# Kernel optimization log

Hardware: AMD Instinct MI355X
Metric: run time of the kernel (lower is better)

The kernel has to match this reference:

```python
import jax, jax.numpy as jnp
import numpy as np

C = 256          # n_channels
D = 32           # head_dim
HEADS = C // D   # 8 heads in the MLA block
EXP = 4          # MBConv expansion
EPS = 1e-15      # attention epsilon
BN_EPS = 1e-5    # BatchNorm eps (eval mode, mean=0, var=1)
BN_SCALE = 1.0 / np.sqrt(1.0 + BN_EPS)


def _hswish(x):
    return x * jnp.clip(x + 3.0, 0.0, 6.0) * (1.0 / 6.0)


def _dwconv(x, w, pad):
    # depthwise conv, NCHW, weight (Cout,1,k,k), groups = Cout
    return jax.lax.conv_general_dilated(
        x, w, (1, 1), [(pad, pad), (pad, pad)],
        feature_group_count=w.shape[0],
        dimension_numbers=('NCHW', 'OIHW', 'NCHW'))


def _bn(x, gamma, beta):
    # eval-mode BN with running_mean=0, running_var=1
    return (gamma * BN_SCALE)[None, :, None, None] * x + beta[None, :, None, None]


def setup_inputs() -> dict:
    key = jax.random.key(0)
    ks = jax.random.split(key, 16)
    s = 0.05
    return {
        'x': jax.random.normal(ks[0], (8, C, 64, 64), jnp.float32),
        'W_qkv': jax.random.normal(ks[1], (3 * C, C), jnp.float32) * s,
        'W_dw5': jax.random.normal(ks[2], (3 * C, 1, 5, 5), jnp.float32) * s,
        'W_pw': jax.random.normal(ks[3], (3 * HEADS, D, D), jnp.float32) * s,
        'W_proj': jax.random.normal(ks[4], (C, 2 * C), jnp.float32) * s,
        'g_proj': jnp.ones((C,), jnp.float32),
        'b_proj': jnp.zeros((C,), jnp.float32),
        'W_e': jax.random.normal(ks[5], (EXP * C, C), jnp.float32) * s,
        'b_e': jax.random.normal(ks[6], (EXP * C,), jnp.float32) * s,
        'W_dw3': jax.random.normal(ks[7], (EXP * C, 1, 3, 3), jnp.float32) * s,
        'b_dw3': jax.random.normal(ks[8], (EXP * C,), jnp.float32) * s,
        'W_p': jax.random.normal(ks[9], (C, EXP * C), jnp.float32) * s,
        'g_p': jnp.ones((C,), jnp.float32),
        'b_p': jnp.zeros((C,), jnp.float32),
    }


def reference(x, W_qkv, W_dw5, W_pw, W_proj, g_proj, b_proj,
              W_e, b_e, W_dw3, b_dw3, W_p, g_p, b_p):
    B, _, H, W = x.shape
    # --- LightweightMLABlock ---
    qkv = jnp.einsum('oi,bihw->bohw', W_qkv, x)                 # (B,3C,H,W)
    # multi-scale aggregator: dw5x5 -> grouped 1x1 (groups=3*HEADS, 32x32 each)
    ag = _dwconv(qkv, W_dw5, 2)
    ag = ag.reshape(B, 3 * HEADS, D, H, W)
    ag = jnp.einsum('ged,bgdhw->bgehw', W_pw, ag).reshape(B, 3 * C, H, W)
    qkv_cat = jnp.concatenate([qkv, ag], axis=1)                # (B,6C,H,W)
    # ReLU linear attention (H*W=4096 > D=32 -> linear branch)
    N = H * W
    t = qkv_cat.reshape(B, 2 * HEADS, 3 * D, N)
    q = jax.nn.relu(t[:, :, :D])
    k = jax.nn.relu(t[:, :, D:2 * D])
    v = t[:, :, 2 * D:]
    vpad = jnp.concatenate([v, jnp.ones((B, 2 * HEADS, 1, N), v.dtype)], axis=2)
    vk = jnp.einsum('bhdn,bhen->bhde', vpad, k)                 # (B,h,D+1,D)
    out = jnp.einsum('bhde,bhen->bhdn', vk, q)                  # (B,h,D+1,N)
    out = out[:, :, :D] / (out[:, :, D:] + EPS)
    att = out.reshape(B, 2 * C, H, W)
    proj = _bn(jnp.einsum('oi,bihw->bohw', W_proj, att), g_proj, b_proj)
    y = proj + x                                                # attention residual
    # --- MobileBottleneckBlock ---
    e = _hswish(jnp.einsum('oi,bihw->bohw', W_e, y) + b_e[None, :, None, None])
    d = _hswish(_dwconv(e, W_dw3, 1) + b_dw3[None, :, None, None])
    p = _bn(jnp.einsum('oi,bihw->bohw', W_p, d), g_p, b_p)
    return p + y                                                # MBConv residual
```

## Files before the change

### kernel.cpp

```cpp
#include <hip/hip_runtime.h>

typedef __bf16 bf16;
typedef __attribute__((ext_vector_type(8))) __bf16 bf16x8;
typedef __attribute__((ext_vector_type(4))) __bf16 bf16x4;
typedef __attribute__((ext_vector_type(2))) __bf16 bf16x2;
typedef __attribute__((ext_vector_type(4))) float f32x4;
typedef __attribute__((ext_vector_type(2))) float f32x2;

static constexpr int NPIX = 4096;
static constexpr float BN_SC = 0.9999950000374997f;
static constexpr float ATT_EPS = 1e-15f;

__device__ __forceinline__ float hswish_f(float v) {
  return v * fminf(fmaxf(v + 3.0f, 0.0f), 6.0f) * (1.0f / 6.0f);
}

__device__ __forceinline__ void gload16(const void* g, void* l) {
  __builtin_amdgcn_global_load_lds(
      (const __attribute__((address_space(1))) unsigned int*)g,
      (__attribute__((address_space(3))) unsigned int*)l, 16, 0, 0);
}

__device__ __forceinline__ float b2f_lo(unsigned int u) {
  union { unsigned int i; float f; } v; v.i = u << 16; return v.f;
}
__device__ __forceinline__ float b2f_hi(unsigned int u) {
  union { unsigned int i; float f; } v; v.i = u & 0xffff0000u; return v.f;
}
__device__ __forceinline__ unsigned short f2b_u(float f) {
  union { float f; unsigned int i; } v; v.f = f;
  unsigned int r = v.i + 0x7FFFu + ((v.i >> 16) & 1u);
  return (unsigned short)(r >> 16);
}

__global__ __launch_bounds__(256)
void x_to_nhwc(const float* __restrict__ x, bf16* __restrict__ xn) {
  __shared__ float t[32][65];
  const int img = blockIdx.z;
  const int n0 = blockIdx.x * 64, c0 = blockIdx.y * 32;
  const int tid = threadIdx.x;
  const float* xb = x + ((size_t)img * 256 + c0) * NPIX + n0;
  {
    const int col = tid & 63, r0 = tid >> 6;
#pragma unroll
    for (int i = 0; i < 8; ++i) {
      const int r = r0 + i * 4;
      t[r][col] = xb[(size_t)r * NPIX + col];
    }
  }
  __syncthreads();
  const int n = tid & 63, cq = tid >> 6;
  bf16x8 v;
#pragma unroll
  for (int j = 0; j < 8; ++j) v[j] = (bf16)t[cq * 8 + j][n];
  *(bf16x8*)(xn + ((size_t)img * NPIX + n0 + n) * 256 + c0 + cq * 8) = v;
}

__global__ void wcvt3(const float* __restrict__ W_proj, const float* __restrict__ W_e,
                      const float* __restrict__ W_p, bf16* __restrict__ o_proj,
                      bf16* __restrict__ o_e, bf16* __restrict__ o_p) {
  const int i = blockIdx.x * 256 + threadIdx.x;
  if (i < 131072) o_proj[i] = (bf16)W_proj[i];
  else if (i < 393216) o_e[i - 131072] = (bf16)W_e[i - 131072];
  else o_p[i - 393216] = (bf16)W_p[i - 393216];
}

__global__ void wqkv_perm(const float* __restrict__ w, bf16* __restrict__ o) {
  const int row = blockIdx.x;
  const int t = row >> 8, r = row & 255, h = r >> 5, d = r & 31;
  const int oldrow = h * 96 + t * 32 + d;
  o[row * 256 + threadIdx.x] = (bf16)w[oldrow * 256 + threadIdx.x];
}

template<int EPI>
__global__ __launch_bounds__(256, 3)
void mfma_gemm(const bf16* __restrict__ A, const bf16* __restrict__ Bact,
               bf16* __restrict__ Yb, float* __restrict__ Yf,
               const int M, const int K,
               const float* __restrict__ p0, const float* __restrict__ p1,
               const bf16* __restrict__ res)
{
  __shared__ __attribute__((aligned(16))) char ldsA[16384];
  __shared__ __attribute__((aligned(16))) char ldsB[16384];
  const int img = blockIdx.z;
  const int n0 = blockIdx.x * 128;
  const int m0 = blockIdx.y * 128;
  const bf16* Bi = Bact + (size_t)img * NPIX * K;
  const int tid = threadIdx.x;
  const int w = tid >> 6, l = tid & 63;
  const int g = l >> 4, ln = l & 15;
  const int wr = w >> 1, wc = w & 1;
  const int lrow = l >> 3;
  const int sofs = (((l & 7) ^ lrow) << 4);

  f32x4 acc[4][4];
#pragma unroll
  for (int i = 0; i < 4; ++i)
#pragma unroll
    for (int j = 0; j < 4; ++j) acc[i][j] = (f32x4){0.f, 0.f, 0.f, 0.f};

  const char* Abase = (const char*)(A + (size_t)m0 * K);
  const char* Bbase = (const char*)(Bi + (size_t)n0 * K);
  const size_t rowb = (size_t)K * 2;
  const int swz = (ln & 7) << 4;

  const int nk = K >> 6;
  for (int kt = 0; kt < nk; ++kt) {
    const int k0b = kt << 7;
#pragma unroll
    for (int i = 0; i < 4; ++i) {
      const int q = (w << 2) + i;
      const int r = q * 8 + lrow;
      gload16(Abase + (size_t)r * rowb + k0b + sofs, ldsA + q * 1024);
    }
#pragma unroll
    for (int i = 0; i < 4; ++i) {
      const int q = (w << 2) + i;
      const int r = q * 8 + lrow;
      gload16(Bbase + (size_t)r * rowb + k0b + sofs, ldsB + q * 1024);
    }
    __syncthreads();
#pragma unroll
    for (int kk = 0; kk < 2; ++kk) {
      bf16x8 av[4], bv[4];
#pragma unroll
      for (int f = 0; f < 4; ++f) {
        const int ra = wr * 64 + f * 16 + ln;
        const int rb = wc * 64 + f * 16 + ln;
        const int kb = kk * 64 + (g << 4);
        av[f] = *(const bf16x8*)(ldsA + ra * 128 + (kb ^ swz));
        bv[f] = *(const bf16x8*)(ldsB + rb * 128 + (kb ^ swz));
      }
#pragma unroll
      for (int fi = 0; fi < 4; ++fi)
#pragma unroll
        for (int fj = 0; fj < 4; ++fj)
          acc[fi][fj] = __builtin_amdgcn_mfma_f32_16x16x32_bf16(
              av[fi], bv[fj], acc[fi][fj], 0, 0, 0);
    }
    __syncthreads();
  }

#pragma unroll
  for (int fi = 0; fi < 4; ++fi) {
    const int m4 = m0 + wr * 64 + fi * 16 + g * 4;
    f32x4 P0 = {0.f, 0.f, 0.f, 0.f}, P1 = {0.f, 0.f, 0.f, 0.f};
    if (EPI == 1 || EPI == 3) { P0 = *(const f32x4*)(p0 + m4); P1 = *(const f32x4*)(p1 + m4); }
    if (EPI == 2) { P0 = *(const f32x4*)(p0 + m4); }
#pragma unroll
    for (int fj = 0; fj < 4; ++fj) {
      const int n = n0 + wc * 64 + fj * 16 + ln;
      if (EPI == 3) {
        const bf16x4 yr = *(const bf16x4*)(res + ((size_t)img * NPIX + n) * 256 + m4);
        float* op = Yf + ((size_t)img * 256 + m4) * NPIX + n;
#pragma unroll
        for (int r = 0; r < 4; ++r)
          op[(size_t)r * NPIX] = P0[r] * BN_SC * acc[fi][fj][r] + P1[r] + (float)yr[r];
      } else {
        bf16x4 sv;
        if (EPI == 0) {
#pragma unroll
          for (int r = 0; r < 4; ++r) sv[r] = (bf16)acc[fi][fj][r];
        } else if (EPI == 1) {
          const bf16x4 xr = *(const bf16x4*)(res + ((size_t)img * NPIX + n) * 256 + m4);
#pragma unroll
          for (int r = 0; r < 4; ++r)
            sv[r] = (bf16)(P0[r] * BN_SC * acc[fi][fj][r] + P1[r] + (float)xr[r]);
        } else {
#pragma unroll
          for (int r = 0; r < 4; ++r)
            sv[r] = (bf16)hswish_f(acc[fi][fj][r] + P0[r]);
        }
        *(bf16x4*)(Yb + ((size_t)img * NPIX + n) * M + m4) = sv;
      }
    }
  }
}

__global__ __launch_bounds__(512)
void dw5pw_nhwc(const bf16* __restrict__ qkv, const float* __restrict__ W5,
                const float* __restrict__ Wpw, bf16* __restrict__ ag) {
  const int gch = blockIdx.y, img = blockIdx.z;
  const int t_ = gch >> 3, hh_ = gch & 7;
  const int n0 = blockIdx.x * 256;
  const int r0 = n0 >> 6;
  __shared__ __attribute__((aligned(16))) unsigned int sInT[16 * 548];
  __shared__ __attribute__((aligned(16))) unsigned int sS32[256 * 20];
  __shared__ __attribute__((aligned(16))) bf16 sPw[32 * 32];
  const int tid = threadIdx.x;
  for (int i = tid; i < 1024; i += 512) sPw[i] = (bf16)Wpw[(hh_ * 3 + t_) * 1024 + i];
  for (int i = tid; i < 2176; i += 512) {
    const int s = i & 3, hp = i >> 2;
    const int hr = hp / 68, hc = hp - hr * 68;
    const int gr = r0 + hr - 2, gc = hc - 2;
    uint4 vv = {0u, 0u, 0u, 0u};
    if (gr >= 0 && gr < 64 && gc >= 0 && gc < 64)
      vv = *(const uint4*)(qkv + ((size_t)img * NPIX + gr * 64 + gc) * 768 + gch * 32 + s * 8);
    unsigned int* rp = sInT + (s * 4) * 548 + hp;
    rp[0] = vv.x; rp[548] = vv.y; rp[1096] = vv.z; rp[1644] = vv.w;
  }
  const int ci = tid & 15;
  f32x2 w2[25];
  {
    const float* wp0 = W5 + (size_t)(hh_ * 96 + t_ * 32 + 2 * ci) * 25;
#pragma unroll
    for (int q = 0; q < 25; ++q) w2[q] = (f32x2){wp0[q], wp0[25 + q]};
  }
  __syncthreads();
  {
    const int pg = tid >> 4;
    const int p0 = pg * 8;
    const int prow = p0 >> 6, pcol = p0 & 63;
    f32x2 a2[8];
#pragma unroll
    for (int px = 0; px < 8; ++px) a2[px] = (f32x2){0.f, 0.f};
#pragma unroll
    for (int ky = 0; ky < 5; ++ky) {
      const unsigned int* wp = &sInT[ci * 548 + (prow + ky) * 68 + pcol];
      const uint4 qa = *(const uint4*)wp;
      const uint4 qb = *(const uint4*)(wp + 4);
      const uint4 qc = *(const uint4*)(wp + 8);
      const unsigned int win[12] = {qa.x, qa.y, qa.z, qa.w, qb.x, qb.y, qb.z, qb.w,
                                    qc.x, qc.y, qc.z, qc.w};
      f32x2 val[12];
#pragma unroll
      for (int j = 0; j < 12; ++j) val[j] = (f32x2){b2f_lo(win[j]), b2f_hi(win[j])};
#pragma unroll
      for (int px = 0; px < 8; ++px)
#pragma unroll
        for (int kx = 0; kx < 5; ++kx)
          a2[px] = val[px + kx] * w2[ky * 5 + kx] + a2[px];
    }
#pragma unroll
    for (int px = 0; px < 8; ++px) {
      const unsigned int pk = (unsigned int)f2b_u(a2[px][0]) | ((unsigned int)f2b_u(a2[px][1]) << 16);
      sS32[(p0 + px) * 20 + ci] = pk;
    }
  }
  __syncthreads();
  {
    const int w = tid >> 6, l = tid & 63;
    const int lg = l >> 4, ln = l & 15;
    f32x4 acc[2][2];
#pragma unroll
    for (int i = 0; i < 2; ++i)
#pragma unroll
      for (int j = 0; j < 2; ++j) acc[i][j] = (f32x4){0.f, 0.f, 0.f, 0.f};
    bf16x8 av[2], bv[2];
#pragma unroll
    for (int et = 0; et < 2; ++et)
      av[et] = *(const bf16x8*)((const char*)sPw + (et * 16 + ln) * 64 + lg * 16);
#pragma unroll
    for (int pt = 0; pt < 2; ++pt)
      bv[pt] = *(const bf16x8*)((const char*)sS32 + ((2 * w + pt) * 16 + ln) * 80 + lg * 16);
#pragma unroll
    for (int et = 0; et < 2; ++et)
#pragma unroll
      for (int pt = 0; pt < 2; ++pt)
        acc[et][pt] = __builtin_amdgcn_mfma_f32_16x16x32_bf16(av[et], bv[pt], acc[et][pt], 0, 0, 0);
#pragma unroll
    for (int et = 0; et < 2; ++et)
#pragma unroll
      for (int pt = 0; pt < 2; ++pt) {
        const int e0 = et * 16 + lg * 4;
        const int p = n0 + (2 * w + pt) * 16 + ln;
        bf16x4 sv;
#pragma unroll
        for (int r = 0; r < 4; ++r) sv[r] = (bf16)acc[et][pt][r];
        *(bf16x4*)(ag + ((size_t)img * NPIX + p) * 768 + gch * 32 + e0) = sv;
      }
  }
}

__global__ __launch_bounds__(256)
void vk_part(const bf16* __restrict__ qkv, const bf16* __restrict__ ag,
             float* __restrict__ partial) {
  const int chunk = blockIdx.x, src = blockIdx.y, img = blockIdx.z;
  const bf16* base = (src == 0 ? qkv : ag) + (size_t)img * NPIX * 768 + 256;
  __shared__ __attribute__((aligned(16))) char tile[32 * 1024];
  const int tid = threadIdx.x;
  const int e2 = tid & 15, sd = tid >> 4;
  const int spx = tid >> 3, sseg = tid & 7;
  float acc[8][2][2] = {};
  float accd[8][2] = {};
  for (int sub = 0; sub < 4; ++sub) {
    __syncthreads();
    {
      const int px0 = chunk * 128 + sub * 32;
      const char* gp = (const char*)(base + (size_t)(px0 + spx) * 768) + sseg * 128;
      char* lp = tile + spx * 1024;
      const int swz = (spx & 7) << 4;
#pragma unroll
      for (int i = 0; i < 8; ++i) {
        const uint4 v = *(const uint4*)(gp + i * 16);
        *(uint4*)(lp + ((sseg * 128 + i * 16) ^ swz)) = v;
      }
    }
    __syncthreads();
    for (int nn = 0; nn < 32; ++nn) {
      const char* row = tile + nn * 1024;
      const int swzn = (nn & 7) << 4;
#pragma unroll
      for (int h = 0; h < 8; ++h) {
        const unsigned int kk = *(const unsigned int*)(row + ((h * 64 + e2 * 4) ^ swzn));
        const float k0 = fmaxf(b2f_lo(kk), 0.f), k1 = fmaxf(b2f_hi(kk), 0.f);
        const unsigned int vv = *(const unsigned int*)(row + ((512 + h * 64 + sd * 4) ^ swzn));
        const float v0 = b2f_lo(vv), v1 = b2f_hi(vv);
        acc[h][0][0] = fmaf(v0, k0, acc[h][0][0]);
        acc[h][0][1] = fmaf(v0, k1, acc[h][0][1]);
        acc[h][1][0] = fmaf(v1, k0, acc[h][1][0]);
        acc[h][1][1] = fmaf(v1, k1, acc[h][1][1]);
        accd[h][0] += k0; accd[h][1] += k1;
      }
    }
  }
  float* pb = partial + ((size_t)((img * 2 + src) * 32 + chunk)) * 8448;
#pragma unroll
  for (int h = 0; h < 8; ++h) {
#pragma unroll
    for (int dj = 0; dj < 2; ++dj)
#pragma unroll
      for (int ej = 0; ej < 2; ++ej)
        pb[h * 1056 + (sd * 2 + dj) * 32 + e2 * 2 + ej] = acc[h][dj][ej];
    if (sd == 0) {
      pb[h * 1056 + 1024 + e2 * 2]     = accd[h][0];
      pb[h * 1056 + 1024 + e2 * 2 + 1] = accd[h][1];
    }
  }
}

__global__ __launch_bounds__(256)
void vk_reduce(const float* __restrict__ partial, bf16* __restrict__ svkT,
               float* __restrict__ dvec) {
  const int h = blockIdx.x & 15, img = blockIdx.x >> 4;
  const int tid = threadIdx.x;
  const int e = tid & 31, dq = tid >> 5;
  const int src = h >> 3, hh = h & 7;
  const float* pb = partial + (size_t)((img * 2 + src) * 32) * 8448 + hh * 1056;
  float a[4] = {};
  for (int c = 0; c < 32; ++c) {
    const float* pc = pb + (size_t)c * 8448;
#pragma unroll
    for (int j = 0; j < 4; ++j) a[j] += pc[(dq * 4 + j) * 32 + e];
  }
  bf16x4 o;
#pragma unroll
  for (int j = 0; j < 4; ++j) o[j] = (bf16)a[j];
  *(bf16x4*)(svkT + (((size_t)img * 16 + h) * 32 + e) * 32 + dq * 4) = o;
  if (dq == 0) {
    float ds = 0.f;
    for (int c = 0; c < 32; ++c) ds += pb[(size_t)c * 8448 + 1024 + e];
    dvec[((size_t)img * 16 + h) * 32 + e] = ds;
  }
}

__global__ __launch_bounds__(256)
void att_pix(const bf16* __restrict__ qkv, const bf16* __restrict__ ag,
             const bf16* __restrict__ svkT, const float* __restrict__ dvec,
             bf16* __restrict__ att) {
  const int pc = blockIdx.x;
  const int img = blockIdx.z;
  __shared__ float sq[8][516];
  __shared__ __attribute__((aligned(16))) bf16 ssvk[16 * 1024];
  __shared__ float sdv[16 * 32];
  const int tid = threadIdx.x;
  const int px0 = pc * 8;
  {
    const int px = tid >> 5, part = tid & 31;
    const bf16* srcp = (part < 16 ? qkv : ag) + (size_t)(img * NPIX + px0 + px) * 768 + (part & 15) * 16;
    const bf16x8 v0 = *(const bf16x8*)srcp;
    const bf16x8 v1 = *(const bf16x8*)(srcp + 8);
    const int c0 = (part < 16 ? 0 : 256) + (part & 15) * 16;
#pragma unroll
    for (int j = 0; j < 8; ++j) {
      sq[px][c0 + j]     = fmaxf((float)v0[j], 0.f);
      sq[px][c0 + 8 + j] = fmaxf((float)v1[j], 0.f);
    }
  }
  {
    const bf16* sb = svkT + (size_t)img * 16384;
    for (int i = tid; i < 2048; i += 256)
      *(bf16x8*)(ssvk + i * 8) = *(const bf16x8*)(sb + i * 8);
    const float* db = dvec + (size_t)img * 512;
    for (int i = tid; i < 512; i += 256) sdv[i] = db[i];
  }
  __syncthreads();
  const int s = tid & 31, px = tid >> 5;
  const int shalf = s >> 4, sd = s & 15, d0 = sd * 2;
  const unsigned int* sv32 = (const unsigned int*)ssvk;
  bf16* ob = att + (size_t)(img * NPIX + px0 + px) * 512;
#pragma unroll
  for (int hh = 0; hh < 8; ++hh) {
    const int h = shalf * 8 + hh;
    const float* qp = &sq[px][h * 32];
    const unsigned int* kp = sv32 + h * 512 + sd;
    const float* dp = &sdv[h * 32];
    float a0 = 0.f, a1 = 0.f, den = 0.f;
#pragma unroll
    for (int ee = 0; ee < 32; ++ee) {
      const float qf = qp[ee];
      const unsigned int wv = kp[ee * 16];
      a0 = fmaf(qf, b2f_lo(wv), a0);
      a1 = fmaf(qf, b2f_hi(wv), a1);
      den = fmaf(qf, dp[ee], den);
    }
    const float inv = 1.f / (den + ATT_EPS);
    bf16x2 o; o[0] = (bf16)(a0 * inv); o[1] = (bf16)(a1 * inv);
    *(bf16x2*)(ob + h * 32 + d0) = o;
  }
}

__global__ __launch_bounds__(256)
void dw3_nhwc(const bf16* __restrict__ ein, const float* __restrict__ w3,
              const float* __restrict__ bias, bf16* __restrict__ dout) {
  const int idx = blockIdx.x * 256 + threadIdx.x;
  const int c8 = idx & 127;
  const int seg = idx >> 7;
  const int img = seg >> 8;
  const int p0 = (seg & 255) * 16;
  const int ch = c8 * 8;
  float wr_[9][8];
#pragma unroll
  for (int j = 0; j < 8; ++j)
#pragma unroll
    for (int q = 0; q < 9; ++q) wr_[q][j] = w3[(ch + j) * 9 + q];
  const f32x4 b0 = *(const f32x4*)(bias + ch), b1 = *(const f32x4*)(bias + ch + 4);
  const int row = p0 >> 6, col0 = p0 & 63;
  const bf16* ib = ein + (size_t)img * NPIX * 1024 + ch;
  bf16* ob = dout + (size_t)img * NPIX * 1024 + ch;
  for (int pp = 0; pp < 16; ++pp) {
    const int col = col0 + pp;
    float a[8] = {b0[0], b0[1], b0[2], b0[3], b1[0], b1[1], b1[2], b1[3]};
#pragma unroll
    for (int ky = 0; ky < 3; ++ky) {
      const int r = row + ky - 1;
      if (r < 0 || r > 63) continue;
#pragma unroll
      for (int kx = 0; kx < 3; ++kx) {
        const int cc = col + kx - 1;
        if (cc < 0 || cc > 63) continue;
        const bf16x8 v = *(const bf16x8*)(ib + (size_t)(r * 64 + cc) * 1024);
#pragma unroll
        for (int j = 0; j < 8; ++j) a[j] += wr_[ky * 3 + kx][j] * (float)v[j];
      }
    }
    bf16x8 o;
#pragma unroll
    for (int j = 0; j < 8; ++j) o[j] = (bf16)hswish_f(a[j]);
    *(bf16x8*)(ob + (size_t)(row * 64 + col) * 1024) = o;
  }
}

extern "C" void kernel_launch(void* const* d_in, const int* in_sizes, int n_in,
                              void* d_out, int out_size, void* d_ws, size_t ws_size,
                              hipStream_t stream) {
  const float* x      = (const float*)d_in[0];
  const float* W_qkv  = (const float*)d_in[1];
  const float* W_dw5  = (const float*)d_in[2];
  const float* W_pw   = (const float*)d_in[3];
  const float* W_proj = (const float*)d_in[4];
  const float* g_proj = (const float*)d_in[5];
  const float* b_proj = (const float*)d_in[6];
  const float* W_e    = (const float*)d_in[7];
  const float* b_e    = (const float*)d_in[8];
  const float* W_dw3  = (const float*)d_in[9];
  const float* b_dw3  = (const float*)d_in[10];
  const float* W_p    = (const float*)d_in[11];
  const float* g_p    = (const float*)d_in[12];
  const float* b_p    = (const float*)d_in[13];
  float* out = (float*)d_out;

  int nb = 8;
  while (nb > 1) {
    size_t need = (size_t)nb * 23169024ull + 1703936ull + 1024;
    if (need <= ws_size) break;
    nb >>= 1;
  }

  char* p = (char*)d_ws;
  float* partial = (float*)p;                 p += (size_t)nb * 2162688;
  float* dvec    = (float*)p;                 p += (size_t)nb * 2048;
  bf16* wq_bf    = (bf16*)p;                  p += 196608ull * 2;
  bf16* wproj_bf = (bf16*)p;                  p += 131072ull * 2;
  bf16* we_bf    = (bf16*)p;                  p += 262144ull * 2;
  bf16* wp_bf    = (bf16*)p;                  p += 262144ull * 2;
  bf16* svkT     = (bf16*)p;                  p += (size_t)nb * 32768;
  bf16* arena    = (bf16*)p;
  bf16* xn   = arena;
  bf16* qkvb = arena + (size_t)nb * 1048576;
  bf16* agb  = qkvb + (size_t)nb * 3145728;
  bf16* attb = agb + (size_t)nb * 3145728;
  bf16* yb   = attb + (size_t)nb * 2097152;
  bf16* eb   = qkvb;
  bf16* db   = qkvb + (size_t)nb * 4194304;

  wqkv_perm<<<768, 256, 0, stream>>>(W_qkv, wq_bf);
  wcvt3<<<2560, 256, 0, stream>>>(W_proj, W_e, W_p, wproj_bf, we_bf, wp_bf);

  for (int b0 = 0; b0 < 8; b0 += nb) {
    const float* x_c = x + (size_t)b0 * 256 * NPIX;
    float* out_c = out + (size_t)b0 * 256 * NPIX;

    x_to_nhwc<<<dim3(64, 8, nb), 256, 0, stream>>>(x_c, xn);
    mfma_gemm<0><<<dim3(32, 6, nb), 256, 0, stream>>>(wq_bf, xn, qkvb, nullptr,
                                                      768, 256, nullptr, nullptr, nullptr);
    dw5pw_nhwc<<<dim3(16, 24, nb), 512, 0, stream>>>(qkvb, W_dw5, W_pw, agb);
    vk_part<<<dim3(32, 2, nb), 256, 0, stream>>>(qkvb, agb, partial);
    vk_reduce<<<nb * 16, 256, 0, stream>>>(partial, svkT, dvec);
    att_pix<<<dim3(512, 1, nb), 256, 0, stream>>>(qkvb, agb, svkT, dvec, attb);
    mfma_gemm<1><<<dim3(32, 2, nb), 256, 0, stream>>>(wproj_bf, attb, yb, nullptr,
                                                      256, 512, g_proj, b_proj, xn);
    mfma_gemm<2><<<dim3(32, 8, nb), 256, 0, stream>>>(we_bf, yb, eb, nullptr,
                                                      1024, 256, b_e, nullptr, nullptr);
    dw3_nhwc<<<nb * 128, 256, 0, stream>>>(eb, W_dw3, b_dw3, db);
    mfma_gemm<3><<<dim3(32, 2, nb), 256, 0, stream>>>(wp_bf, db, nullptr, out_c,
                                                      256, 1024, g_p, b_p, yb);
  }
}
```

Measured before the change: 405.3 us.

## Retile vk_part register blocking and keep q in bf16 in att_pix

vk_part now gives each wave one head and has each thread compute a 4x8 tile of the v·k outer product with packed f32x2 FMAs, which reuses each LDS load more. ReLU on k is applied once during the global-to-LDS copy via a bit-mask trick. The chunk count doubles to 64 for more blocks, which doubles the partial buffer and the reduce loop length. att_pix keeps q as ReLU'd packed bf16 in LDS, processes 16 pixels per block with 16 threads each looping over all heads, and halves the grid size.

Measured after the change: 365.3 us. -9.9%, faster.

```diff
diff --git a/kernel.cpp b/kernel.cpp
--- a/kernel.cpp
+++ b/kernel.cpp
@@ -31,6 +31,11 @@
   union { float f; unsigned int i; } v; v.f = f;
   unsigned int r = v.i + 0x7FFFu + ((v.i >> 16) & 1u);
   return (unsigned short)(r >> 16);
+}
+__device__ __forceinline__ unsigned int relu2(unsigned int v) {
+  const unsigned int s = v & 0x80008000u;
+  const unsigned int m = (s >> 15) * 0xFFFFu;
+  return v & ~m;
 }
 
 __global__ __launch_bounds__(256)
@@ -279,20 +284,30 @@
   const bf16* base = (src == 0 ? qkv : ag) + (size_t)img * NPIX * 768 + 256;
   __shared__ __attribute__((aligned(16))) char tile[32 * 1024];
   const int tid = threadIdx.x;
-  const int e2 = tid & 15, sd = tid >> 4;
+  const int h = tid >> 5;
+  const int r5 = tid & 31;
+  const int et = r5 & 3;
+  const int dq = r5 >> 2;
   const int spx = tid >> 3, sseg = tid & 7;
-  float acc[8][2][2] = {};
-  float accd[8][2] = {};
-  for (int sub = 0; sub < 4; ++sub) {
+  f32x2 acc[4][4];
+#pragma unroll
+  for (int i = 0; i < 4; ++i)
+#pragma unroll
+    for (int j = 0; j < 4; ++j) acc[i][j] = (f32x2){0.f, 0.f};
+  f32x2 dsum[4] = {(f32x2){0.f,0.f},(f32x2){0.f,0.f},(f32x2){0.f,0.f},(f32x2){0.f,0.f}};
+  for (int sub = 0; sub < 2; ++sub) {
     __syncthreads();
     {
-      const int px0 = chunk * 128 + sub * 32;
+      const int px0 = chunk * 64 + sub * 32;
       const char* gp = (const char*)(base + (size_t)(px0 + spx) * 768) + sseg * 128;
       char* lp = tile + spx * 1024;
       const int swz = (spx & 7) << 4;
 #pragma unroll
       for (int i = 0; i < 8; ++i) {
-        const uint4 v = *(const uint4*)(gp + i * 16);
+        uint4 v = *(const uint4*)(gp + i * 16);
+        if (sseg < 4) {
+          v.x = relu2(v.x); v.y = relu2(v.y); v.z = relu2(v.z); v.w = relu2(v.w);
+        }
         *(uint4*)(lp + ((sseg * 128 + i * 16) ^ swz)) = v;
       }
     }
@@ -300,31 +315,41 @@
     for (int nn = 0; nn < 32; ++nn) {
       const char* row = tile + nn * 1024;
       const int swzn = (nn & 7) << 4;
-#pragma unroll
-      for (int h = 0; h < 8; ++h) {
-        const unsigned int kk = *(const unsigned int*)(row + ((h * 64 + e2 * 4) ^ swzn));
-        const float k0 = fmaxf(b2f_lo(kk), 0.f), k1 = fmaxf(b2f_hi(kk), 0.f);
-        const unsigned int vv = *(const unsigned int*)(row + ((512 + h * 64 + sd * 4) ^ swzn));
-        const float v0 = b2f_lo(vv), v1 = b2f_hi(vv);
-        acc[h][0][0] = fmaf(v0, k0, acc[h][0][0]);
-        acc[h][0][1] = fmaf(v0, k1, acc[h][0][1]);
-        acc[h][1][0] = fmaf(v1, k0, acc[h][1][0]);
-        acc[h][1][1] = fmaf(v1, k1, acc[h][1][1]);
-        accd[h][0] += k0; accd[h][1] += k1;
-      }
-    }
-  }
-  float* pb = partial + ((size_t)((img * 2 + src) * 32 + chunk)) * 8448;
-#pragma unroll
-  for (int h = 0; h < 8; ++h) {
-#pragma unroll
-    for (int dj = 0; dj < 2; ++dj)
-#pragma unroll
-      for (int ej = 0; ej < 2; ++ej)
-        pb[h * 1056 + (sd * 2 + dj) * 32 + e2 * 2 + ej] = acc[h][dj][ej];
-    if (sd == 0) {
-      pb[h * 1056 + 1024 + e2 * 2]     = accd[h][0];
-      pb[h * 1056 + 1024 + e2 * 2 + 1] = accd[h][1];
+      f32x2 kp[4];
+#pragma unroll
+      for (int j = 0; j < 4; ++j) {
+        const unsigned int kk = *(const unsigned int*)(row + ((h * 64 + (et * 4 + j) * 4) ^ swzn));
+        kp[j] = (f32x2){b2f_lo(kk), b2f_hi(kk)};
+      }
+      const unsigned int v0 = *(const unsigned int*)(row + ((512 + h * 64 + dq * 8) ^ swzn));
+      const unsigned int v1 = *(const unsigned int*)(row + ((512 + h * 64 + dq * 8 + 4) ^ swzn));
+      const float vd[4] = {b2f_lo(v0), b2f_hi(v0), b2f_lo(v1), b2f_hi(v1)};
+#pragma unroll
+      for (int i = 0; i < 4; ++i)
+#pragma unroll
+        for (int j = 0; j < 4; ++j)
+          acc[i][j] = (f32x2){vd[i], vd[i]} * kp[j] + acc[i][j];
+      if (dq == 0) {
+#pragma unroll
+        for (int j = 0; j < 4; ++j) dsum[j] = dsum[j] + kp[j];
+      }
+    }
+  }
+  float* pb = partial + ((size_t)((img * 2 + src) * 64 + chunk)) * 8448;
+#pragma unroll
+  for (int i = 0; i < 4; ++i) {
+    const int d = dq * 4 + i;
+#pragma unroll
+    for (int j = 0; j < 4; ++j) {
+      pb[h * 1056 + d * 32 + et * 8 + j * 2]     = acc[i][j][0];
+      pb[h * 1056 + d * 32 + et * 8 + j * 2 + 1] = acc[i][j][1];
+    }
+  }
+  if (dq == 0) {
+#pragma unroll
+    for (int j = 0; j < 4; ++j) {
+      pb[h * 1056 + 1024 + et * 8 + j * 2]     = dsum[j][0];
+      pb[h * 1056 + 1024 + et * 8 + j * 2 + 1] = dsum[j][1];
     }
   }
 }
@@ -336,9 +361,9 @@
   const int tid = threadIdx.x;
   const int e = tid & 31, dq = tid >> 5;
   const int src = h >> 3, hh = h & 7;
-  const float* pb = partial + (size_t)((img * 2 + src) * 32) * 8448 + hh * 1056;
+  const float* pb = partial + (size_t)((img * 2 + src) * 64) * 8448 + hh * 1056;
   float a[4] = {};
-  for (int c = 0; c < 32; ++c) {
+  for (int c = 0; c < 64; ++c) {
     const float* pc = pb + (size_t)c * 8448;
 #pragma unroll
     for (int j = 0; j < 4; ++j) a[j] += pc[(dq * 4 + j) * 32 + e];
@@ -349,7 +374,7 @@
   *(bf16x4*)(svkT + (((size_t)img * 16 + h) * 32 + e) * 32 + dq * 4) = o;
   if (dq == 0) {
     float ds = 0.f;
-    for (int c = 0; c < 32; ++c) ds += pb[(size_t)c * 8448 + 1024 + e];
+    for (int c = 0; c < 64; ++c) ds += pb[(size_t)c * 8448 + 1024 + e];
     dvec[((size_t)img * 16 + h) * 32 + e] = ds;
   }
 }
@@ -360,21 +385,19 @@
              bf16* __restrict__ att) {
   const int pc = blockIdx.x;
   const int img = blockIdx.z;
-  __shared__ float sq[8][516];
+  __shared__ __attribute__((aligned(16))) unsigned int squ[16][264];
   __shared__ __attribute__((aligned(16))) bf16 ssvk[16 * 1024];
-  __shared__ float sdv[16 * 32];
+  __shared__ float sdv[512];
   const int tid = threadIdx.x;
-  const int px0 = pc * 8;
+  const int px0 = pc * 16;
+  const int px = tid >> 4, s = tid & 15;
   {
-    const int px = tid >> 5, part = tid & 31;
-    const bf16* srcp = (part < 16 ? qkv : ag) + (size_t)(img * NPIX + px0 + px) * 768 + (part & 15) * 16;
-    const bf16x8 v0 = *(const bf16x8*)srcp;
-    const bf16x8 v1 = *(const bf16x8*)(srcp + 8);
-    const int c0 = (part < 16 ? 0 : 256) + (part & 15) * 16;
-#pragma unroll
-    for (int j = 0; j < 8; ++j) {
-      sq[px][c0 + j]     = fmaxf((float)v0[j], 0.f);
-      sq[px][c0 + 8 + j] = fmaxf((float)v1[j], 0.f);
+    const bf16* srcp = (s < 8 ? qkv : ag) + (size_t)(img * NPIX + px0 + px) * 768 + (s & 7) * 32;
+#pragma unroll
+    for (int i = 0; i < 4; ++i) {
+      uint4 v = *(const uint4*)((const char*)srcp + i * 16);
+      v.x = relu2(v.x); v.y = relu2(v.y); v.z = relu2(v.z); v.w = relu2(v.w);
+      *(uint4*)&squ[px][s * 16 + i * 4] = v;
     }
   }
   {
@@ -385,24 +408,24 @@
     for (int i = tid; i < 512; i += 256) sdv[i] = db[i];
   }
   __syncthreads();
-  const int s = tid & 31, px = tid >> 5;
-  const int shalf = s >> 4, sd = s & 15, d0 = sd * 2;
+  const int sd = s, d0 = sd * 2;
   const unsigned int* sv32 = (const unsigned int*)ssvk;
   bf16* ob = att + (size_t)(img * NPIX + px0 + px) * 512;
 #pragma unroll
-  for (int hh = 0; hh < 8; ++hh) {
-    const int h = shalf * 8 + hh;
-    const float* qp = &sq[px][h * 32];
+  for (int h = 0; h < 16; ++h) {
+    const unsigned int* qp = &squ[px][h * 16];
     const unsigned int* kp = sv32 + h * 512 + sd;
     const float* dp = &sdv[h * 32];
     float a0 = 0.f, a1 = 0.f, den = 0.f;
 #pragma unroll
-    for (int ee = 0; ee < 32; ++ee) {
-      const float qf = qp[ee];
-      const unsigned int wv = kp[ee * 16];
-      a0 = fmaf(qf, b2f_lo(wv), a0);
-      a1 = fmaf(qf, b2f_hi(wv), a1);
-      den = fmaf(qf, dp[ee], den);
+    for (int e2 = 0; e2 < 16; ++e2) {
+      const unsigned int qq = qp[e2];
+      const float q0 = b2f_lo(qq), q1 = b2f_hi(qq);
+      const unsigned int w0 = kp[(2 * e2) * 16];
+      const unsigned int w1 = kp[(2 * e2 + 1) * 16];
+      a0 = fmaf(q0, b2f_lo(w0), a0); a0 = fmaf(q1, b2f_lo(w1), a0);
+      a1 = fmaf(q0, b2f_hi(w0), a1); a1 = fmaf(q1, b2f_hi(w1), a1);
+      den = fmaf(q0, dp[2 * e2], den); den = fmaf(q1, dp[2 * e2 + 1], den);
     }
     const float inv = 1.f / (den + ATT_EPS);
     bf16x2 o; o[0] = (bf16)(a0 * inv); o[1] = (bf16)(a1 * inv);
@@ -472,13 +495,13 @@
 
   int nb = 8;
   while (nb > 1) {
-    size_t need = (size_t)nb * 23169024ull + 1703936ull + 1024;
+    size_t need = (size_t)nb * 25331712ull + 1703936ull + 1024;
     if (need <= ws_size) break;
     nb >>= 1;
   }
 
   char* p = (char*)d_ws;
-  float* partial = (float*)p;                 p += (size_t)nb * 2162688;
+  float* partial = (float*)p;                 p += (size_t)nb * 4325376;
   float* dvec    = (float*)p;                 p += (size_t)nb * 2048;
   bf16* wq_bf    = (bf16*)p;                  p += 196608ull * 2;
   bf16* wproj_bf = (bf16*)p;                  p += 131072ull * 2;
@@ -505,9 +528,9 @@
     mfma_gemm<0><<<dim3(32, 6, nb), 256, 0, stream>>>(wq_bf, xn, qkvb, nullptr,
                                                       768, 256, nullptr, nullptr, nullptr);
     dw5pw_nhwc<<<dim3(16, 24, nb), 512, 0, stream>>>(qkvb, W_dw5, W_pw, agb);
-    vk_part<<<dim3(32, 2, nb), 256, 0, stream>>>(qkvb, agb, partial);
+    vk_part<<<dim3(64, 2, nb), 256, 0, stream>>>(qkvb, agb, partial);
     vk_reduce<<<nb * 16, 256, 0, stream>>>(partial, svkT, dvec);
-    att_pix<<<dim3(512, 1, nb), 256, 0, stream>>>(qkvb, agb, svkT, dvec, attb);
+    att_pix<<<dim3(256, 1, nb), 256, 0, stream>>>(qkvb, agb, svkT, dvec, attb);
     mfma_gemm<1><<<dim3(32, 2, nb), 256, 0, stream>>>(wproj_bf, attb, yb, nullptr,
                                                       256, 512, g_proj, b_proj, xn);
     mfma_gemm<2><<<dim3(32, 8, nb), 256, 0, stream>>>(we_bf, yb, eb, nullptr,
```
